# Kernel tuning notes

Measured on AMD Instinct MI355X. Metric: run time of the kernel, lower is better.

## Reference

```python
import jax, jax.numpy as jnp
import numpy as np

T = 1.0  # temperature (default in original forward)


def setup_inputs() -> dict:
    key = jax.random.key(0)
    k1, k2 = jax.random.split(key)
    N, M, D = 65536, 512, 256
    z = jax.random.normal(k1, (N, D), dtype=jnp.float32)
    e = jax.random.normal(k2, (M, D), dtype=jnp.float32)
    log_sigma = jnp.zeros((1,), dtype=jnp.float32)  # init_log_sigma = 0.0
    return {"z": z, "e": e, "log_sigma": log_sigma}


def reference(z, e, log_sigma):
    N, z_dim = z.shape
    M = e.shape[0]
    # pad N up to a multiple of M (zeros), then view as [B, M, z_dim]
    N_pad = ((N + M - 1) // M) * M
    z = jnp.pad(z, ((0, N_pad - N), (0, 0)))
    zb = z.reshape(-1, M, z_dim)  # [B, M, D]
    # squared euclidean distance via GEMM form: ||z||^2 + ||e||^2 - 2 z.e -> [B, M, M]
    dist = (
        jnp.sum(zb * zb, axis=-1)[:, :, None]
        + jnp.sum(e * e, axis=-1)[None, None, :]
        - 2.0 * jnp.einsum("bmd,kd->bmk", zb, e)
    )
    alpha = -1.0 / (2.0 * jnp.exp(log_sigma[0]) ** 2)
    # logsumexp over the z-block dim (axis=1), mean over codebook dim (axis=1 after reduce)
    loss = -jnp.mean(T * jax.nn.logsumexp(alpha * dist / T, axis=1), axis=1)  # [B]
    loss = loss + 0.5 * z_dim * (2.0 * log_sigma[0] - 1.0) + jnp.log(jnp.float32(M))
    return jnp.mean(loss)
```

## Files before the change

kernel.cpp:

```cpp
#include <hip/hip_runtime.h>
#include <stdint.h>
#include <math.h>

typedef __attribute__((ext_vector_type(8))) short short8;
typedef __attribute__((ext_vector_type(16))) float f32x16;

#define DEVI static __device__ __forceinline__

constexpr int D = 256;

constexpr size_t WS_EIMG  = 0;
constexpr size_t WS_ETERM = 262144;
constexpr size_t WS_WMAX  = 264192;
constexpr size_t WS_WSUM  = WS_WMAX + 524288;
constexpr size_t WS_PART  = WS_WSUM + 524288;

DEVI unsigned int f2bf(float f) {
  unsigned int u = __float_as_uint(f);
  return (u + 0x7fffu + ((u >> 16) & 1u)) >> 16;
}
DEVI float shflx(float v, int m) { return __shfl_xor(v, m, 64); }

__global__ void prep_e(const float* __restrict__ e, const float* __restrict__ lsp,
                       char* __restrict__ eimg, float* __restrict__ eterm) {
  const int et = blockIdx.x, t = threadIdx.x;
  const int c = t >> 3, o = t & 7;
  const int gc = et * 32 + c;
  const float a = __expf(-2.0f * lsp[0]);
  const float* s = e + (size_t)gc * D + o * 32;
  float sq = 0.0f;
  unsigned int w[16];
#pragma unroll
  for (int i = 0; i < 8; ++i) {
    float4 x = *(const float4*)(s + i * 4);
    sq += x.x * x.x + x.y * x.y + x.z * x.z + x.w * x.w;
    w[2 * i]     = f2bf(a * x.x) | (f2bf(a * x.y) << 16);
    w[2 * i + 1] = f2bf(a * x.z) | (f2bf(a * x.w) << 16);
  }
  sq += shflx(sq, 1); sq += shflx(sq, 2); sq += shflx(sq, 4);
  char* base = eimg + (size_t)et * 16384;
#pragma unroll
  for (int i = 0; i < 4; ++i) {
    int g = o * 4 + i;
    int phys = (g >> 1) * 1024 + (g & 1) * 512 + c * 16;
    uint4 pk; pk.x = w[4 * i]; pk.y = w[4 * i + 1];
    pk.z = w[4 * i + 2]; pk.w = w[4 * i + 3];
    *(uint4*)(base + phys) = pk;
  }
  if (o == 0) eterm[gc] = -0.5f * a * sq;
}

__global__ __launch_bounds__(1024, 4)
void lse_main(const float* __restrict__ z, const char* __restrict__ eimg,
              const float* __restrict__ lsp, float* __restrict__ wmax,
              float* __restrict__ wsum) {
  __shared__ char  zbuf[2][16384];
  __shared__ float ztm[2][32];

  const int tid = threadIdx.x;
  const int wid = tid >> 6, lane = tid & 63;
  const int l31 = lane & 31;
  const int hi  = lane >> 5;
  const int n_st = tid >> 5;
  const int g_st = tid & 31;
  const int bx = blockIdx.x;
  const float a = __expf(-2.0f * lsp[0]);
  const float* zrow = z + ((size_t)bx * 256 + n_st) * D + g_st * 8;

  float4 zr0 = *(const float4*)(zrow);
  float4 zr1 = *(const float4*)(zrow + 4);

  short8 A[16];
#pragma unroll
  for (int s = 0; s < 16; ++s)
    A[s] = *(const short8*)(eimg + wid * 16384 + s * 1024 + lane * 16);

  auto COMMIT = [&](int buf, float4 x0, float4 x1) {
    float sq = x0.x * x0.x + x0.y * x0.y + x0.z * x0.z + x0.w * x0.w +
               x1.x * x1.x + x1.y * x1.y + x1.z * x1.z + x1.w * x1.w;
    sq += shflx(sq, 1); sq += shflx(sq, 2); sq += shflx(sq, 4);
    sq += shflx(sq, 8); sq += shflx(sq, 16);
    uint4 pk;
    pk.x = f2bf(x0.x) | (f2bf(x0.y) << 16);
    pk.y = f2bf(x0.z) | (f2bf(x0.w) << 16);
    pk.z = f2bf(x1.x) | (f2bf(x1.y) << 16);
    pk.w = f2bf(x1.z) | (f2bf(x1.w) << 16);
    *(uint4*)(&zbuf[buf][0] + n_st * 512 + ((g_st ^ n_st) * 16)) = pk;
    if ((tid & 31) == 0) ztm[buf][n_st] = -0.5f * a * sq;
  };

  COMMIT(0, zr0, zr1);
  __syncthreads();

  float mx = -1e30f;
  float sm[16];
#pragma unroll
  for (int r = 0; r < 16; ++r) sm[r] = 0.0f;

  for (int c = 0; c < 8; ++c) {
    const int cur = c & 1;
    if (c < 7) {
      const float* src = zrow + (size_t)(c + 1) * 32 * D;
      zr0 = *(const float4*)(src);
      zr1 = *(const float4*)(src + 4);
    }

    f32x16 acc;
#pragma unroll
    for (int i = 0; i < 16; ++i) acc[i] = 0.0f;
#pragma unroll
    for (int s = 0; s < 16; ++s) {
      short8 B = *(const short8*)(&zbuf[cur][0] + l31 * 512 +
                                  (((2 * s + hi) ^ l31) * 16));
      acc = __builtin_amdgcn_mfma_f32_32x32x16_bf16(A[s], B, acc, 0, 0, 0);
    }

    const float zt = ztm[cur][l31];
    float vmax = acc[0];
#pragma unroll
    for (int r = 1; r < 16; ++r) vmax = fmaxf(vmax, acc[r]);
    vmax += zt;
    const float nm = fmaxf(mx, vmax);
    const float sc = __expf(mx - nm);
    const float tz = zt - nm;
#pragma unroll
    for (int r = 0; r < 16; ++r) sm[r] = sm[r] * sc + __expf(acc[r] + tz);
    mx = nm;

    if (c < 7) COMMIT(cur ^ 1, zr0, zr1);
    __syncthreads();
  }

  float MX = mx;
  MX = fmaxf(MX, shflx(MX, 1));  MX = fmaxf(MX, shflx(MX, 2));
  MX = fmaxf(MX, shflx(MX, 4));  MX = fmaxf(MX, shflx(MX, 8));
  MX = fmaxf(MX, shflx(MX, 16));
  const float sc = __expf(mx - MX);
#pragma unroll
  for (int r = 0; r < 16; ++r) {
    float t = sm[r] * sc;
    t += shflx(t, 1); t += shflx(t, 2); t += shflx(t, 4);
    t += shflx(t, 8); t += shflx(t, 16);
    sm[r] = t;
  }
  if (l31 == 0) {
#pragma unroll
    for (int r = 0; r < 16; ++r) {
      const int col = wid * 32 + (r & 3) + 8 * (r >> 2) + 4 * hi;
      wmax[(size_t)bx * 512 + col] = MX;
      wsum[(size_t)bx * 512 + col] = sm[r];
    }
  }
}

__global__ void merge_b(const float* __restrict__ wmax, const float* __restrict__ wsum,
                        const float* __restrict__ eterm, float* __restrict__ partial) {
  __shared__ float sh[512];
  const int b = blockIdx.x, t = threadIdx.x;
  float m0 = wmax[(size_t)(2 * b) * 512 + t];
  float m1 = wmax[(size_t)(2 * b + 1) * 512 + t];
  float s0 = wsum[(size_t)(2 * b) * 512 + t];
  float s1 = wsum[(size_t)(2 * b + 1) * 512 + t];
  float nm = fmaxf(m0, m1);
  float s = s0 * __expf(m0 - nm) + s1 * __expf(m1 - nm);
  sh[t] = nm + logf(s) + eterm[t];
  __syncthreads();
  for (int st = 256; st > 0; st >>= 1) {
    if (t < st) sh[t] += sh[t + st];
    __syncthreads();
  }
  if (t == 0) partial[b] = sh[0];
}

__global__ void final_k(const float* __restrict__ partial,
                        const float* __restrict__ lsp, float* __restrict__ out) {
  __shared__ float sh[128];
  const int t = threadIdx.x;
  sh[t] = partial[t];
  __syncthreads();
  for (int st = 64; st > 0; st >>= 1) {
    if (t < st) sh[t] += sh[t + st];
    __syncthreads();
  }
  if (t == 0) {
    float ls = lsp[0];
    out[0] = -sh[0] / 65536.0f + 128.0f * (2.0f * ls - 1.0f) + logf(512.0f);
  }
}

extern "C" void kernel_launch(void* const* d_in, const int* in_sizes, int n_in,
                              void* d_out, int out_size, void* d_ws, size_t ws_size,
                              hipStream_t stream) {
  const float* z   = (const float*)d_in[0];
  const float* e   = (const float*)d_in[1];
  const float* lsp = (const float*)d_in[2];
  float* out = (float*)d_out;
  char* ws = (char*)d_ws;
  char*  eimg    = ws + WS_EIMG;
  float* eterm   = (float*)(ws + WS_ETERM);
  float* wmax    = (float*)(ws + WS_WMAX);
  float* wsum    = (float*)(ws + WS_WSUM);
  float* partial = (float*)(ws + WS_PART);

  prep_e<<<dim3(16), dim3(256), 0, stream>>>(e, lsp, eimg, eterm);
  lse_main<<<dim3(256), dim3(1024), 0, stream>>>(z, eimg, lsp, wmax, wsum);
  merge_b<<<dim3(128), dim3(512), 0, stream>>>(wmax, wsum, eterm, partial);
  final_k<<<dim3(1), dim3(128), 0, stream>>>(partial, lsp, out);
}
```

Baseline: 48.89 us.

## Process 64-row z chunks with split prefetch, base-2 exponentials and lazy rescaling

Folds log2(e) into the e-image and z-norm terms so the online logsumexp uses exp2 directly instead of __expf. The z loop now stages 64-row chunks in two 32-row halves, interleaving global loads and bf16 commits with the MFMA work and halving the number of block barriers. The running-max rescale is skipped when no lane's max grows, and s_setprio raises wave priority around the MFMA loops. This doubles LDS use per block, which may cut occupancy, and adds a wave-wide vote on every update.

```diff
diff --git a/kernel.cpp b/kernel.cpp
--- a/kernel.cpp
+++ b/kernel.cpp
@@ -8,6 +8,8 @@
 #define DEVI static __device__ __forceinline__
 
 constexpr int D = 256;
+constexpr float LOG2E = 1.4426950408889634f;
+constexpr float LN2   = 0.6931471805599453f;
 
 constexpr size_t WS_EIMG  = 0;
 constexpr size_t WS_ETERM = 262144;
@@ -27,6 +29,7 @@
   const int c = t >> 3, o = t & 7;
   const int gc = et * 32 + c;
   const float a = __expf(-2.0f * lsp[0]);
+  const float sab = a * LOG2E;
   const float* s = e + (size_t)gc * D + o * 32;
   float sq = 0.0f;
   unsigned int w[16];
@@ -34,8 +37,8 @@
   for (int i = 0; i < 8; ++i) {
     float4 x = *(const float4*)(s + i * 4);
     sq += x.x * x.x + x.y * x.y + x.z * x.z + x.w * x.w;
-    w[2 * i]     = f2bf(a * x.x) | (f2bf(a * x.y) << 16);
-    w[2 * i + 1] = f2bf(a * x.z) | (f2bf(a * x.w) << 16);
+    w[2 * i]     = f2bf(sab * x.x) | (f2bf(sab * x.y) << 16);
+    w[2 * i + 1] = f2bf(sab * x.z) | (f2bf(sab * x.w) << 16);
   }
   sq += shflx(sq, 1); sq += shflx(sq, 2); sq += shflx(sq, 4);
   char* base = eimg + (size_t)et * 16384;
@@ -54,8 +57,8 @@
 void lse_main(const float* __restrict__ z, const char* __restrict__ eimg,
               const float* __restrict__ lsp, float* __restrict__ wmax,
               float* __restrict__ wsum) {
-  __shared__ char  zbuf[2][16384];
-  __shared__ float ztm[2][32];
+  __shared__ char  zbuf[2][32768];
+  __shared__ float ztm[2][64];
 
   const int tid = threadIdx.x;
   const int wid = tid >> 6, lane = tid & 63;
@@ -65,31 +68,37 @@
   const int g_st = tid & 31;
   const int bx = blockIdx.x;
   const float a = __expf(-2.0f * lsp[0]);
+  const float ztf = -0.5f * a * LOG2E;
   const float* zrow = z + ((size_t)bx * 256 + n_st) * D + g_st * 8;
 
-  float4 zr0 = *(const float4*)(zrow);
-  float4 zr1 = *(const float4*)(zrow + 4);
-
-  short8 A[16];
-#pragma unroll
-  for (int s = 0; s < 16; ++s)
-    A[s] = *(const short8*)(eimg + wid * 16384 + s * 1024 + lane * 16);
-
-  auto COMMIT = [&](int buf, float4 x0, float4 x1) {
-    float sq = x0.x * x0.x + x0.y * x0.y + x0.z * x0.z + x0.w * x0.w +
-               x1.x * x1.x + x1.y * x1.y + x1.z * x1.z + x1.w * x1.w;
+  float4 zr0, zr1;
+  auto ISSUE = [&](int c, int sub) {
+    const float* src = zrow + (size_t)(c * 64 + sub * 32) * D;
+    zr0 = *(const float4*)(src);
+    zr1 = *(const float4*)(src + 4);
+  };
+  auto COMMIT = [&](int buf, int sub) {
+    float sq = zr0.x * zr0.x + zr0.y * zr0.y + zr0.z * zr0.z + zr0.w * zr0.w +
+               zr1.x * zr1.x + zr1.y * zr1.y + zr1.z * zr1.z + zr1.w * zr1.w;
     sq += shflx(sq, 1); sq += shflx(sq, 2); sq += shflx(sq, 4);
     sq += shflx(sq, 8); sq += shflx(sq, 16);
     uint4 pk;
-    pk.x = f2bf(x0.x) | (f2bf(x0.y) << 16);
-    pk.y = f2bf(x0.z) | (f2bf(x0.w) << 16);
-    pk.z = f2bf(x1.x) | (f2bf(x1.y) << 16);
-    pk.w = f2bf(x1.z) | (f2bf(x1.w) << 16);
-    *(uint4*)(&zbuf[buf][0] + n_st * 512 + ((g_st ^ n_st) * 16)) = pk;
-    if ((tid & 31) == 0) ztm[buf][n_st] = -0.5f * a * sq;
+    pk.x = f2bf(zr0.x) | (f2bf(zr0.y) << 16);
+    pk.y = f2bf(zr0.z) | (f2bf(zr0.w) << 16);
+    pk.z = f2bf(zr1.x) | (f2bf(zr1.y) << 16);
+    pk.w = f2bf(zr1.z) | (f2bf(zr1.w) << 16);
+    *(uint4*)(&zbuf[buf][0] + (sub * 32 + n_st) * 512 + ((g_st ^ n_st) * 16)) = pk;
+    if (g_st == 0) ztm[buf][sub * 32 + n_st] = ztf * sq;
   };
 
-  COMMIT(0, zr0, zr1);
+  ISSUE(0, 0);
+  short8 A[16];
+#pragma unroll
+  for (int s = 0; s < 16; ++s)
+    A[s] = *(const short8*)(eimg + wid * 16384 + s * 1024 + lane * 16);
+  COMMIT(0, 0);
+  ISSUE(0, 1);
+  COMMIT(0, 1);
   __syncthreads();
 
   float mx = -1e30f;
@@ -97,45 +106,68 @@
 #pragma unroll
   for (int r = 0; r < 16; ++r) sm[r] = 0.0f;
 
-  for (int c = 0; c < 8; ++c) {
+  auto UPDATE = [&](f32x16& acc, float zt) {
+    float t0 = fmaxf(fmaxf(acc[0], acc[1]), fmaxf(acc[2], acc[3]));
+    float t1 = fmaxf(fmaxf(acc[4], acc[5]), fmaxf(acc[6], acc[7]));
+    float t2 = fmaxf(fmaxf(acc[8], acc[9]), fmaxf(acc[10], acc[11]));
+    float t3 = fmaxf(fmaxf(acc[12], acc[13]), fmaxf(acc[14], acc[15]));
+    float vmax = fmaxf(fmaxf(t0, t1), fmaxf(t2, t3)) + zt;
+    if (!__all(vmax <= mx)) {
+      float nm = fmaxf(mx, vmax);
+      float sc = exp2f(mx - nm);
+#pragma unroll
+      for (int r = 0; r < 16; ++r) sm[r] *= sc;
+      mx = nm;
+    }
+    const float tz = zt - mx;
+#pragma unroll
+    for (int r = 0; r < 16; ++r) sm[r] += exp2f(acc[r] + tz);
+  };
+
+#pragma unroll
+  for (int c = 0; c < 4; ++c) {
     const int cur = c & 1;
-    if (c < 7) {
-      const float* src = zrow + (size_t)(c + 1) * 32 * D;
-      zr0 = *(const float4*)(src);
-      zr1 = *(const float4*)(src + 4);
-    }
+    const char* bp = &zbuf[cur][0];
+
+    if (c < 3) ISSUE(c + 1, 0);
 
     f32x16 acc;
 #pragma unroll
     for (int i = 0; i < 16; ++i) acc[i] = 0.0f;
+    __builtin_amdgcn_s_setprio(1);
 #pragma unroll
     for (int s = 0; s < 16; ++s) {
-      short8 B = *(const short8*)(&zbuf[cur][0] + l31 * 512 +
+      short8 B = *(const short8*)(bp + l31 * 512 + (((2 * s + hi) ^ l31) * 16));
+      acc = __builtin_amdgcn_mfma_f32_32x32x16_bf16(A[s], B, acc, 0, 0, 0);
+    }
+    __builtin_amdgcn_s_setprio(0);
+    if (c < 3) COMMIT(cur ^ 1, 0);
+    UPDATE(acc, ztm[cur][l31]);
+
+    if (c < 3) ISSUE(c + 1, 1);
+
+    f32x16 acc2;
+#pragma unroll
+    for (int i = 0; i < 16; ++i) acc2[i] = 0.0f;
+    __builtin_amdgcn_s_setprio(1);
+#pragma unroll
+    for (int s = 0; s < 16; ++s) {
+      short8 B = *(const short8*)(bp + (32 + l31) * 512 +
                                   (((2 * s + hi) ^ l31) * 16));
-      acc = __builtin_amdgcn_mfma_f32_32x32x16_bf16(A[s], B, acc, 0, 0, 0);
-    }
-
-    const float zt = ztm[cur][l31];
-    float vmax = acc[0];
-#pragma unroll
-    for (int r = 1; r < 16; ++r) vmax = fmaxf(vmax, acc[r]);
-    vmax += zt;
-    const float nm = fmaxf(mx, vmax);
-    const float sc = __expf(mx - nm);
-    const float tz = zt - nm;
-#pragma unroll
-    for (int r = 0; r < 16; ++r) sm[r] = sm[r] * sc + __expf(acc[r] + tz);
-    mx = nm;
-
-    if (c < 7) COMMIT(cur ^ 1, zr0, zr1);
-    __syncthreads();
+      acc2 = __builtin_amdgcn_mfma_f32_32x32x16_bf16(A[s], B, acc2, 0, 0, 0);
+    }
+    __builtin_amdgcn_s_setprio(0);
+    if (c < 3) COMMIT(cur ^ 1, 1);
+    UPDATE(acc2, ztm[cur][32 + l31]);
+
+    if (c < 3) __syncthreads();
   }
 
   float MX = mx;
   MX = fmaxf(MX, shflx(MX, 1));  MX = fmaxf(MX, shflx(MX, 2));
   MX = fmaxf(MX, shflx(MX, 4));  MX = fmaxf(MX, shflx(MX, 8));
   MX = fmaxf(MX, shflx(MX, 16));
-  const float sc = __expf(mx - MX);
+  const float sc = exp2f(mx - MX);
 #pragma unroll
   for (int r = 0; r < 16; ++r) {
     float t = sm[r] * sc;
@@ -162,8 +194,8 @@
   float s0 = wsum[(size_t)(2 * b) * 512 + t];
   float s1 = wsum[(size_t)(2 * b + 1) * 512 + t];
   float nm = fmaxf(m0, m1);
-  float s = s0 * __expf(m0 - nm) + s1 * __expf(m1 - nm);
-  sh[t] = nm + logf(s) + eterm[t];
+  float s = s0 * exp2f(m0 - nm) + s1 * exp2f(m1 - nm);
+  sh[t] = LN2 * (nm + log2f(s)) + eterm[t];
   __syncthreads();
   for (int st = 256; st > 0; st >>= 1) {
     if (t < st) sh[t] += sh[t + st];
```

New measurement: 76.82 us. 57.1% more time.
